# Kernel optimization log

Measured on AMD Instinct MI355X. Metric: run time of the kernel, lower is better.

The kernel has to match this reference:

```python
import jax, jax.numpy as jnp
import numpy as np

N_HEAD = 16
T_THRESHOLD = 0.001


def setup_inputs() -> dict:
    key = jax.random.key(0)
    k_x, k_wa, k_ba, k_wp, k_bp = jax.random.split(key, 5)
    B, P, L, R = 8, 1024, 4, 256
    C = L * R  # n_embd = 1024
    s = 1.0 / np.sqrt(C)
    return {
        "x": jax.random.normal(k_x, (B, P, L, R), dtype=jnp.float32),
        "w_attn": jax.random.normal(k_wa, (C, 3 * C), dtype=jnp.float32) * s,
        "b_attn": jax.random.normal(k_ba, (3 * C,), dtype=jnp.float32) * 0.01,
        "w_proj": jax.random.normal(k_wp, (C, C), dtype=jnp.float32) * s,
        "b_proj": jax.random.normal(k_bp, (C,), dtype=jnp.float32) * 0.01,
    }


def reference(x, w_attn, b_attn, w_proj, b_proj):
    B, P, L, R = x.shape
    C = L * R
    H = N_HEAD
    hd = C // H
    xf = x.reshape(B, P, C)                      # (B, T, C)
    qkv = xf @ w_attn + b_attn                   # (B, T, 3C)
    q, k, v = jnp.split(qkv, 3, axis=-1)
    # (B, H, T, hd)
    q = q.reshape(B, P, H, hd).transpose(0, 2, 1, 3)
    k = k.reshape(B, P, H, hd).transpose(0, 2, 1, 3)
    v = v.reshape(B, P, H, hd).transpose(0, 2, 1, 3)
    att = jnp.einsum("bhqd,bhkd->bhqk", q, k) * (1.0 / np.sqrt(hd))
    att = jax.nn.softmax(att, axis=-1)
    att = jax.nn.relu(att - T_THRESHOLD)         # post-softmax thresholding
    y = jnp.einsum("bhqk,bhkd->bhqd", att, v)    # (B, H, T, hd)
    y = y.transpose(0, 2, 1, 3).reshape(B, P, C)
    y = y @ w_proj + b_proj
    return y.reshape(B, P, L, R)
```

## Files before the change

### kernel.cpp

```cpp
#include <hip/hip_runtime.h>


typedef _Float16 half8 __attribute__((ext_vector_type(8)));
typedef _Float16 half4_t __attribute__((ext_vector_type(4)));
typedef float floatx4 __attribute__((ext_vector_type(4)));

__device__ __forceinline__ void gl2lds16(const void* gsrc, void* lds) {
    __builtin_amdgcn_global_load_lds(
        (const __attribute__((address_space(1))) unsigned int*)gsrc,
        (__attribute__((address_space(3))) unsigned int*)lds,
        16, 0, 0);
}

__global__ __launch_bounds__(256) void conv_x(const float4* __restrict__ in,
                                              _Float16* __restrict__ out, int n4) {
    int idx = blockIdx.x * blockDim.x + threadIdx.x;
    int stride = gridDim.x * blockDim.x;
    for (int i = idx; i < n4; i += stride) {
        float4 v = in[i];
        half4_t h = { (_Float16)v.x, (_Float16)v.y, (_Float16)v.z, (_Float16)v.w };
        *(half4_t*)(out + (size_t)i * 4) = h;
    }
}

__global__ __launch_bounds__(256) void tconv(const float* __restrict__ in,
                                             _Float16* __restrict__ out, int R, int C) {
    __shared__ _Float16 t[64 * 65];
    int bx = blockIdx.x, by = blockIdx.y;
#pragma unroll
    for (int it = 0; it < 16; ++it) {
        int idx = it * 256 + threadIdx.x;
        int r = idx >> 6, c = idx & 63;
        t[c * 65 + r] = (_Float16)in[(size_t)(by * 64 + r) * C + bx * 64 + c];
    }
    __syncthreads();
#pragma unroll
    for (int it = 0; it < 16; ++it) {
        int idx = it * 256 + threadIdx.x;
        int rn = idx >> 6, ck = idx & 63;
        out[(size_t)(bx * 64 + rn) * R + by * 64 + ck] = t[rn * 65 + ck];
    }
}

__global__ __launch_bounds__(256) void pack_k(const _Float16* __restrict__ kn,
                                              _Float16* __restrict__ kP) {
    int cid = blockIdx.x * 256 + threadIdx.x;
    int lane = cid & 63, half = (cid >> 6) & 1, kb = (cid >> 7) & 63, bh = cid >> 13;
    int l15 = lane & 15, quad = lane >> 4;
    int b = bh >> 4, h = bh & 15;
    int t = kb * 16 + l15, d = half * 32 + quad * 8;
    half8 v = *(const half8*)(kn + (size_t)(b * 1024 + t) * 1024 + h * 64 + d);
    *(half8*)(kP + (size_t)cid * 8) = v;
}

__global__ __launch_bounds__(256) void pack_v(const _Float16* __restrict__ vn,
                                              _Float16* __restrict__ vP) {
    __shared__ _Float16 s[32][72];
    int kbv = blockIdx.x, bh = blockIdx.y;
    int b = bh >> 4, h = bh & 15;
    int tid = threadIdx.x;
    {
        int row = tid >> 3, piece = tid & 7;
        *(half8*)&s[row][piece * 8] =
            *(const half8*)(vn + (size_t)(b * 1024 + kbv * 32 + row) * 1024 + h * 64 + piece * 8);
    }
    __syncthreads();
    {
        int l15v = tid & 15, quad = (tid >> 4) & 3, cf = tid >> 6;
        half8 o;
#pragma unroll
        for (int j = 0; j < 8; ++j) o[j] = s[quad * 8 + j][cf * 16 + l15v];
        *(half8*)(vP + ((size_t)(bh * 32 + kbv) * 256 + tid) * 8) = o;
    }
}

template <bool SPLIT3>
__global__ __launch_bounds__(256) void gemm_tn(const _Float16* __restrict__ A,
                                               const _Float16* __restrict__ BT,
                                               const float* __restrict__ bias,
                                               void* __restrict__ o0, void* __restrict__ o1,
                                               void* __restrict__ o2, int N) {
    constexpr int K = 1024;
    __shared__ __attribute__((aligned(16))) _Float16 sA[128 * 32];
    __shared__ __attribute__((aligned(16))) _Float16 sB[128 * 32];
    int tid = threadIdx.x;
    int W = tid >> 6, lane = tid & 63, quad = lane >> 4, l15 = lane & 15;
    int m0 = blockIdx.y * 128, n0 = blockIdx.x * 128;
    int wr = (W >> 1) * 64, wc = (W & 1) * 64;
    floatx4 acc[4][4] = {};

    for (int kt = 0; kt < K / 32; ++kt) {
        int k0 = kt * 32;
#pragma unroll
        for (int rho = 0; rho < 2; ++rho) {
            int lin = rho * 256 + tid;
            const _Float16* gA = A + (size_t)(m0 + (lin >> 2)) * K + k0 + (lin & 3) * 8;
            const _Float16* gB = BT + (size_t)(n0 + (lin >> 2)) * K + k0 + (lin & 3) * 8;
            int ldsoff = __builtin_amdgcn_readfirstlane((rho * 256 + W * 64) * 16);
            gl2lds16(gA, (char*)sA + ldsoff);
            gl2lds16(gB, (char*)sB + ldsoff);
        }
        __syncthreads();
        half8 a[4], b[4];
#pragma unroll
        for (int rf = 0; rf < 4; ++rf)
            a[rf] = *(const half8*)(sA + (wr + rf * 16 + l15) * 32 + quad * 8);
#pragma unroll
        for (int cf = 0; cf < 4; ++cf)
            b[cf] = *(const half8*)(sB + (wc + cf * 16 + l15) * 32 + quad * 8);
#pragma unroll
        for (int rf = 0; rf < 4; ++rf)
#pragma unroll
            for (int cf = 0; cf < 4; ++cf)
                acc[rf][cf] = __builtin_amdgcn_mfma_f32_16x16x32_f16(a[rf], b[cf], acc[rf][cf], 0, 0, 0);
        __syncthreads();
    }
    _Float16* hbase = nullptr;
    if (SPLIT3) {
        int sec = n0 >> 10;
        hbase = (_Float16*)(sec == 0 ? o0 : (sec == 1 ? o1 : o2));
    }
#pragma unroll
    for (int cf = 0; cf < 4; ++cf) {
        int gn = n0 + wc + cf * 16 + l15;
        float bv = bias[gn];
        int cn = gn & 1023;
#pragma unroll
        for (int rf = 0; rf < 4; ++rf) {
            int gmBase = m0 + wr + rf * 16 + quad * 4;
#pragma unroll
            for (int r = 0; r < 4; ++r) {
                float v = acc[rf][cf][r] + bv;
                if (SPLIT3) hbase[(size_t)(gmBase + r) * 1024 + cn] = (_Float16)v;
                else        ((float*)o0)[(size_t)(gmBase + r) * N + gn] = v;
            }
        }
    }
}

__device__ __forceinline__ int esw(int row, int colByte) {
    return row * 2048 + (colByte ^ ((row & 7) << 4));
}

__global__ __launch_bounds__(512, 4) void attn(const _Float16* __restrict__ qn,
                                               const _Float16* __restrict__ kP,
                                               const _Float16* __restrict__ vP,
                                               _Float16* __restrict__ y) {
    __shared__ __attribute__((aligned(16))) _Float16 E[32 * 1024];
    __shared__ float lsum[8][32];
    char* Eb = (char*)E;
    int tid = threadIdx.x;
    int W = tid >> 6, lane = tid & 63, quad = lane >> 4, l15 = lane & 15;
    int qt = blockIdx.x, bh = blockIdx.y;
    int b = bh >> 4, h = bh & 15;
    int q0 = qt * 32;

    half8 bq[2][2];
#pragma unroll
    for (int nf = 0; nf < 2; ++nf)
#pragma unroll
        for (int ks = 0; ks < 2; ++ks)
            bq[nf][ks] = *(const half8*)(qn + (size_t)(b * 1024 + q0 + nf * 16 + l15) * 1024 +
                                         h * 64 + ks * 32 + quad * 8);

    float lpart[2] = {0.f, 0.f};
#pragma unroll 4
    for (int mt = 0; mt < 8; ++mt) {
        int kb = W * 8 + mt;
        const _Float16* kp = kP + ((size_t)(bh * 64 + kb) * 128 + lane) * 8;
        half8 ak0 = *(const half8*)(kp);
        half8 ak1 = *(const half8*)(kp + 512);
#pragma unroll
        for (int nf = 0; nf < 2; ++nf) {
            floatx4 s = {};
            s = __builtin_amdgcn_mfma_f32_16x16x32_f16(ak0, bq[nf][0], s, 0, 0, 0);
            s = __builtin_amdgcn_mfma_f32_16x16x32_f16(ak1, bq[nf][1], s, 0, 0, 0);
            half4_t h4;
#pragma unroll
            for (int r = 0; r < 4; ++r) {
                float e = __expf(fminf(s[r] * 0.125f, 10.0f));
                lpart[nf] += e;
                h4[r] = (_Float16)e;
            }
            int q = nf * 16 + l15;
            int kbyte = (W * 128 + mt * 16 + quad * 4) * 2;
            *(half4_t*)(Eb + q * 2048 + (kbyte ^ ((q & 7) << 4))) = h4;
        }
    }
#pragma unroll
    for (int nf = 0; nf < 2; ++nf) {
        lpart[nf] += __shfl_xor(lpart[nf], 16);
        lpart[nf] += __shfl_xor(lpart[nf], 32);
    }
    if (lane < 16) {
        lsum[W][l15] = lpart[0];
        lsum[W][16 + l15] = lpart[1];
    }
    __syncthreads();

    half8 inv8[2], t8, z8;
#pragma unroll
    for (int j = 0; j < 8; ++j) { t8[j] = (_Float16)(-0.001f); z8[j] = (_Float16)0.f; }
#pragma unroll
    for (int rf = 0; rf < 2; ++rf) {
        float l = 0.f;
#pragma unroll
        for (int w = 0; w < 8; ++w) l += lsum[w][rf * 16 + l15];
        _Float16 invh = (_Float16)(1.0f / l);
#pragma unroll
        for (int j = 0; j < 8; ++j) inv8[rf][j] = invh;
    }

    floatx4 acc[2][4] = {};
#pragma unroll
    for (int kt = 0; kt < 4; ++kt) {
        int kk = W * 128 + kt * 32;
        half8 ap[2];
#pragma unroll
        for (int rf = 0; rf < 2; ++rf) {
            ap[rf] = *(const half8*)(Eb + esw(rf * 16 + l15, (kk + quad * 8) * 2));
            ap[rf] = ap[rf] * inv8[rf] + t8;
            ap[rf] = __builtin_elementwise_max(ap[rf], z8);
        }
        const _Float16* vbase = vP + ((size_t)(bh * 32 + (W * 4 + kt)) * 256 + lane) * 8;
        half8 bv[4];
#pragma unroll
        for (int cf = 0; cf < 4; ++cf)
            bv[cf] = *(const half8*)(vbase + cf * 512);
#pragma unroll
        for (int rf = 0; rf < 2; ++rf)
#pragma unroll
            for (int cf = 0; cf < 4; ++cf)
                acc[rf][cf] = __builtin_amdgcn_mfma_f32_16x16x32_f16(ap[rf], bv[cf], acc[rf][cf], 0, 0, 0);
    }
    __syncthreads();

    float* red = (float*)E;
#pragma unroll
    for (int rf = 0; rf < 2; ++rf)
#pragma unroll
        for (int cf = 0; cf < 4; ++cf)
#pragma unroll
            for (int r = 0; r < 4; ++r)
                red[W * 2048 + (rf * 16 + quad * 4 + r) * 64 + cf * 16 + l15] = acc[rf][cf][r];
    __syncthreads();
    {
        int e4 = tid * 4;
        int r = e4 >> 6, c = e4 & 63;
        floatx4 s = {};
#pragma unroll
        for (int w = 0; w < 8; ++w) s += *(const floatx4*)(red + w * 2048 + e4);
        half4_t hv = { (_Float16)s[0], (_Float16)s[1], (_Float16)s[2], (_Float16)s[3] };
        *(half4_t*)(y + (size_t)(b * 1024 + q0 + r) * 1024 + h * 64 + c) = hv;
    }
}

extern "C" void kernel_launch(void* const* d_in, const int* in_sizes, int n_in,
                              void* d_out, int out_size, void* d_ws, size_t ws_size,
                              hipStream_t stream) {
    const float* x  = (const float*)d_in[0];
    const float* wa = (const float*)d_in[1];
    const float* ba = (const float*)d_in[2];
    const float* wp = (const float*)d_in[3];
    const float* bp = (const float*)d_in[4];
    float* out = (float*)d_out;

    char* ws = (char*)d_ws;
    _Float16* xh  = (_Float16*)(ws);
    _Float16* vP  = (_Float16*)(ws);
    _Float16* qn  = (_Float16*)(ws + 16777216);
    _Float16* kn  = (_Float16*)(ws + 33554432);
    _Float16* y   = (_Float16*)(ws + 33554432);
    _Float16* vn  = (_Float16*)(ws + 50331648);
    _Float16* kP  = (_Float16*)(ws + 67108864);
    _Float16* waT = (_Float16*)(ws + 83886080);
    _Float16* wpT = (_Float16*)(ws + 90177536);

    conv_x<<<4096, 256, 0, stream>>>((const float4*)x, xh, 8388608 / 4);
    tconv<<<dim3(48, 16), 256, 0, stream>>>(wa, waT, 1024, 3072);
    tconv<<<dim3(16, 16), 256, 0, stream>>>(wp, wpT, 1024, 1024);
    gemm_tn<true><<<dim3(24, 64), 256, 0, stream>>>(xh, waT, ba, (void*)qn, (void*)kn, (void*)vn, 3072);
    pack_k<<<4096, 256, 0, stream>>>(kn, kP);
    pack_v<<<dim3(32, 128), 256, 0, stream>>>(vn, vP);
    attn<<<dim3(32, 128), 512, 0, stream>>>(qn, kP, vP, y);
    gemm_tn<false><<<dim3(8, 64), 256, 0, stream>>>(y, wpT, bp, (void*)out, nullptr, nullptr, 1024);
}
```

Baseline: 289.2 us.

## Replace GEMM with 256x128 double-buffered, swizzled, 8-wave pingpong kernel

Replaces the simple 128x128 single-buffered GEMM (K-step 32, sync per step) with a 256x128 tile kernel using 512 threads, K-step 64, double-buffered LDS with XOR swizzle, and interleaved global-to-LDS loads with MFMA phases separated by barriers and s_setprio. It aims to hide global load latency, avoid LDS bank conflicts, and raise compute per byte loaded for both the QKV and projection GEMMs. It costs 96KB of LDS per block, which limits occupancy, and relies on a hand-tuned barrier and vmcnt schedule that is fragile. The grid halves in M, which reduces block count for the smaller projection GEMM.

```diff
diff --git a/kernel.cpp b/kernel.cpp
--- a/kernel.cpp
+++ b/kernel.cpp
@@ -74,47 +74,108 @@
     }
 }
 
+
+#define GBAR __builtin_amdgcn_s_barrier()
+#define WLGKM do { asm volatile("s_waitcnt lgkmcnt(0)" ::: "memory"); } while (0)
+#define WVM2  do { asm volatile("s_waitcnt vmcnt(2)"   ::: "memory"); } while (0)
+
+#define LDA(buf, rg)                                                                          \
+    do {                                                                                      \
+        _Pragma("unroll") for (int i = 0; i < 2; ++i) {                                       \
+            int r_ = wm * 64 + ((rg) * 2 + i) * 16 + l15;                                     \
+            _Pragma("unroll") for (int kk = 0; kk < 2; ++kk)                                  \
+                a[i][kk] = *(const half8*)(sA + (buf) * 32768 + r_ * 128 +                    \
+                                           ((((kk << 2) + quad) ^ (r_ & 7)) << 4));           \
+        }                                                                                     \
+    } while (0)
+
+#define LDB(buf, cg, bb)                                                                      \
+    do {                                                                                      \
+        _Pragma("unroll") for (int j = 0; j < 2; ++j) {                                       \
+            int r_ = wn * 64 + ((cg) * 2 + j) * 16 + l15;                                     \
+            _Pragma("unroll") for (int kk = 0; kk < 2; ++kk)                                  \
+                bb[j][kk] = *(const half8*)(sB + (buf) * 16384 + r_ * 128 +                   \
+                                            ((((kk << 2) + quad) ^ (r_ & 7)) << 4));          \
+        }                                                                                     \
+    } while (0)
+
+#define MMA(rg, cg, bb)                                                                       \
+    do {                                                                                      \
+        __builtin_amdgcn_s_setprio(1);                                                        \
+        _Pragma("unroll") for (int kk = 0; kk < 2; ++kk)                                      \
+            _Pragma("unroll") for (int i = 0; i < 2; ++i)                                     \
+                _Pragma("unroll") for (int j = 0; j < 2; ++j)                                  \
+                    acc[(rg) * 2 + i][(cg) * 2 + j] = __builtin_amdgcn_mfma_f32_16x16x32_f16( \
+                        a[i][kk], bb[j][kk], acc[(rg) * 2 + i][(cg) * 2 + j], 0, 0, 0);       \
+        __builtin_amdgcn_s_setprio(0);                                                        \
+    } while (0)
+
 template <bool SPLIT3>
-__global__ __launch_bounds__(256) void gemm_tn(const _Float16* __restrict__ A,
-                                               const _Float16* __restrict__ BT,
-                                               const float* __restrict__ bias,
-                                               void* __restrict__ o0, void* __restrict__ o1,
-                                               void* __restrict__ o2, int N) {
-    constexpr int K = 1024;
-    __shared__ __attribute__((aligned(16))) _Float16 sA[128 * 32];
-    __shared__ __attribute__((aligned(16))) _Float16 sB[128 * 32];
+__global__ __launch_bounds__(512, 2) void gemm8p(const _Float16* __restrict__ A,
+                                                 const _Float16* __restrict__ BT,
+                                                 const float* __restrict__ bias,
+                                                 void* __restrict__ o0, void* __restrict__ o1,
+                                                 void* __restrict__ o2, int N) {
+    __shared__ __attribute__((aligned(16))) char lds[98304];
+    char* sA = lds;
+    char* sB = lds + 65536;
     int tid = threadIdx.x;
     int W = tid >> 6, lane = tid & 63, quad = lane >> 4, l15 = lane & 15;
-    int m0 = blockIdx.y * 128, n0 = blockIdx.x * 128;
-    int wr = (W >> 1) * 64, wc = (W & 1) * 64;
+    int wm = W >> 1, wn = W & 1;
+    int m0 = blockIdx.y * 256, n0 = blockIdx.x * 128;
+
+    auto stA = [&](int buf, int half, int k0) {
+#pragma unroll
+        for (int rnd = 0; rnd < 2; ++rnd) {
+            int c = rnd * 512 + tid;
+            int row = c >> 3;
+            int q = (c & 7) ^ (row & 7);
+            const _Float16* src = A + (size_t)(m0 + half * 128 + row) * 1024 + k0 + q * 8;
+            int off = __builtin_amdgcn_readfirstlane(buf * 32768 + half * 16384 +
+                                                     rnd * 8192 + (W << 10));
+            gl2lds16(src, sA + off);
+        }
+    };
+    auto stB = [&](int buf, int half, int k0) {
+        int row = tid >> 3;
+        int q = (tid & 7) ^ (row & 7);
+        const _Float16* src = BT + (size_t)(n0 + half * 64 + row) * 1024 + k0 + q * 8;
+        int off = __builtin_amdgcn_readfirstlane(buf * 16384 + half * 8192 + (W << 10));
+        gl2lds16(src, sB + off);
+    };
+
+    half8 a[2][2], b0[2][2], b1[2][2];
     floatx4 acc[4][4] = {};
 
-    for (int kt = 0; kt < K / 32; ++kt) {
-        int k0 = kt * 32;
-#pragma unroll
-        for (int rho = 0; rho < 2; ++rho) {
-            int lin = rho * 256 + tid;
-            const _Float16* gA = A + (size_t)(m0 + (lin >> 2)) * K + k0 + (lin & 3) * 8;
-            const _Float16* gB = BT + (size_t)(n0 + (lin >> 2)) * K + k0 + (lin & 3) * 8;
-            int ldsoff = __builtin_amdgcn_readfirstlane((rho * 256 + W * 64) * 16);
-            gl2lds16(gA, (char*)sA + ldsoff);
-            gl2lds16(gB, (char*)sB + ldsoff);
-        }
-        __syncthreads();
-        half8 a[4], b[4];
-#pragma unroll
-        for (int rf = 0; rf < 4; ++rf)
-            a[rf] = *(const half8*)(sA + (wr + rf * 16 + l15) * 32 + quad * 8);
-#pragma unroll
-        for (int cf = 0; cf < 4; ++cf)
-            b[cf] = *(const half8*)(sB + (wc + cf * 16 + l15) * 32 + quad * 8);
-#pragma unroll
-        for (int rf = 0; rf < 4; ++rf)
-#pragma unroll
-            for (int cf = 0; cf < 4; ++cf)
-                acc[rf][cf] = __builtin_amdgcn_mfma_f32_16x16x32_f16(a[rf], b[cf], acc[rf][cf], 0, 0, 0);
-        __syncthreads();
-    }
+    stA(0, 0, 0); stA(0, 1, 0);
+    stB(0, 0, 0); stB(0, 1, 0);
+    stB(1, 0, 64); stB(1, 1, 64);
+    WVM2;
+    GBAR;
+
+#pragma unroll 1
+    for (int t = 0; t < 16; t += 2) {
+        int k1 = (t + 1) << 6;
+        int k2 = ((t + 2) & 15) << 6;
+        int k3 = ((t + 3) & 15) << 6;
+        LDA(0, 0); LDB(0, 0, b0); stA(1, 0, k1);
+        GBAR; WLGKM; MMA(0, 0, b0); GBAR;
+        LDB(0, 1, b1); stA(1, 1, k1);
+        GBAR; WLGKM; MMA(0, 1, b1); GBAR;
+        LDA(0, 1); stB(0, 0, k2);
+        GBAR; WLGKM; MMA(1, 1, b1); GBAR;
+        stB(0, 1, k2); WVM2;
+        GBAR; WLGKM; MMA(1, 0, b0); GBAR;
+        LDA(1, 0); LDB(1, 0, b0); stA(0, 0, k2);
+        GBAR; WLGKM; MMA(0, 0, b0); GBAR;
+        LDB(1, 1, b1); stA(0, 1, k2);
+        GBAR; WLGKM; MMA(0, 1, b1); GBAR;
+        LDA(1, 1); stB(1, 0, k3);
+        GBAR; WLGKM; MMA(1, 1, b1); GBAR;
+        stB(1, 1, k3); WVM2;
+        GBAR; WLGKM; MMA(1, 0, b0); GBAR;
+    }
+
     _Float16* hbase = nullptr;
     if (SPLIT3) {
         int sec = n0 >> 10;
@@ -122,12 +183,12 @@
     }
 #pragma unroll
     for (int cf = 0; cf < 4; ++cf) {
-        int gn = n0 + wc + cf * 16 + l15;
+        int gn = n0 + wn * 64 + cf * 16 + l15;
         float bv = bias[gn];
         int cn = gn & 1023;
 #pragma unroll
         for (int rf = 0; rf < 4; ++rf) {
-            int gmBase = m0 + wr + rf * 16 + quad * 4;
+            int gmBase = m0 + wm * 64 + rf * 16 + quad * 4;
 #pragma unroll
             for (int r = 0; r < 4; ++r) {
                 float v = acc[rf][cf][r] + bv;
@@ -279,9 +340,9 @@
     conv_x<<<4096, 256, 0, stream>>>((const float4*)x, xh, 8388608 / 4);
     tconv<<<dim3(48, 16), 256, 0, stream>>>(wa, waT, 1024, 3072);
     tconv<<<dim3(16, 16), 256, 0, stream>>>(wp, wpT, 1024, 1024);
-    gemm_tn<true><<<dim3(24, 64), 256, 0, stream>>>(xh, waT, ba, (void*)qn, (void*)kn, (void*)vn, 3072);
+    gemm8p<true><<<dim3(24, 32), 512, 0, stream>>>(xh, waT, ba, (void*)qn, (void*)kn, (void*)vn, 3072);
     pack_k<<<4096, 256, 0, stream>>>(kn, kP);
     pack_v<<<dim3(32, 128), 256, 0, stream>>>(vn, vP);
     attn<<<dim3(32, 128), 512, 0, stream>>>(qn, kP, vP, y);
-    gemm_tn<false><<<dim3(8, 64), 256, 0, stream>>>(y, wpT, bp, (void*)out, nullptr, nullptr, 1024);
-}
+    gemm8p<false><<<dim3(8, 32), 512, 0, stream>>>(y, wpT, bp, (void*)out, nullptr, nullptr, 1024);
+}
```

Result: faster. 280.3 us (-3.1%).
